# Optimization experiments

Hardware: AMD Instinct MI355X
Metric: run time of the kernel (lower is better)

The kernel has to match this reference:

```python
import jax, jax.numpy as jnp
import numpy as np

B, T, C = 1, 4096, 2048
NH, HS, NQG = 16, 128, 4          # n_head, head_size, n_query_groups (GQA)
Q_PER_KV = NH // NQG              # 4
QKV_DIM = (NH + 2 * NQG) * HS     # 3072
ROT = HS // 2                     # rotary half-dim = 64


def setup_inputs() -> dict:
    key = jax.random.key(0)
    k0, k1, k2 = jax.random.split(key, 3)
    x = jax.random.normal(k0, (B, T, C), dtype=jnp.float32)
    W_attn = jax.random.normal(k1, (QKV_DIM, C), dtype=jnp.float32) * 0.02
    W_proj = jax.random.normal(k2, (C, C), dtype=jnp.float32) * 0.02
    # RoPE cache: cos/sin of shape (T, head_size/2), flash-attn convention
    inv_freq = 1.0 / (10000.0 ** (jnp.arange(0, HS, 2, dtype=jnp.float32) / HS))
    freqs = jnp.arange(T, dtype=jnp.float32)[:, None] * inv_freq[None, :]
    return {"x": x, "cos": jnp.cos(freqs), "sin": jnp.sin(freqs),
            "W_attn": W_attn, "W_proj": W_proj}


def _apply_rope(t, cos, sin):
    # t: (B, T, H, HS); cos/sin: (T, ROT). Non-interleaved (rotate-half) form.
    x1, x2 = t[..., :ROT], t[..., ROT:]
    c = cos[None, :, None, :]
    s = sin[None, :, None, :]
    return jnp.concatenate([x1 * c - x2 * s, x2 * c + x1 * s], axis=-1)


def reference(x, cos, sin, W_attn, W_proj):
    Bx, Tx, Cx = x.shape
    qkv = jnp.einsum('btc,fc->btf', x, W_attn)                 # (B,T,3072)
    qkv = qkv.reshape(Bx, Tx, NQG, Q_PER_KV + 2, HS)
    q = qkv[:, :, :, :Q_PER_KV, :].reshape(Bx, Tx, NH, HS)     # (B,T,16,128)
    k = qkv[:, :, :, Q_PER_KV, :]                              # (B,T,4,128)
    v = qkv[:, :, :, Q_PER_KV + 1, :]                          # (B,T,4,128)
    q = _apply_rope(q, cos, sin)
    k = _apply_rope(k, cos, sin)
    # GQA: expand kv groups to match query heads (repeat_interleave on head dim)
    k = jnp.repeat(k, Q_PER_KV, axis=2)                        # (B,T,16,128)
    v = jnp.repeat(v, Q_PER_KV, axis=2)
    scale = 1.0 / np.sqrt(HS).astype(np.float32)
    scores = jnp.einsum('bthd,bshd->bhts', q, k) * scale       # (B,H,T,T)
    causal = jnp.tril(jnp.ones((Tx, Tx), dtype=bool))
    scores = jnp.where(causal[None, None], scores, jnp.finfo(scores.dtype).min)
    attn = jax.nn.softmax(scores, axis=-1)
    y = jnp.einsum('bhts,bshd->bthd', attn, v).reshape(Bx, Tx, Cx)
    return jnp.einsum('btc,oc->bto', y, W_proj)
```

## Files before the change

### kernel.cpp

```cpp
#include <hip/hip_runtime.h>
#include <hip/hip_bf16.h>

typedef __hip_bfloat16 bf16;
typedef __attribute__((ext_vector_type(8))) short short8;
typedef __attribute__((ext_vector_type(4))) short short4v;
typedef __attribute__((ext_vector_type(4))) float floatx4;

#define T_SEQ 4096
#define C_DIM 2048
#define NHEAD 16
#define HSZ   128
#define NGRP  4

#define MFMA_BF16(A,B,C) __builtin_amdgcn_mfma_f32_16x16x32_bf16((A),(B),(C),0,0,0)

__device__ __forceinline__ void gld_lds16(const bf16* g, bf16* l) {
  __builtin_amdgcn_global_load_lds(
      (__attribute__((address_space(1))) void*)(g),
      (__attribute__((address_space(3))) void*)(l), 16, 0, 0);
}

__global__ void cvt_kernel(const float* __restrict__ src, bf16* __restrict__ dst, long n)
{
  const long i = ((long)blockIdx.x * blockDim.x + threadIdx.x) * 8;
  if (i >= n) return;
  const float4 a = *(const float4*)(src + i);
  const float4 b = *(const float4*)(src + i + 4);
  bf16 tmp[8];
  tmp[0] = __float2bfloat16(a.x); tmp[1] = __float2bfloat16(a.y);
  tmp[2] = __float2bfloat16(a.z); tmp[3] = __float2bfloat16(a.w);
  tmp[4] = __float2bfloat16(b.x); tmp[5] = __float2bfloat16(b.y);
  tmp[6] = __float2bfloat16(b.z); tmp[7] = __float2bfloat16(b.w);
  *(short8*)(dst + i) = *(const short8*)tmp;
}

__global__ __launch_bounds__(256, 3)
void gemm_bt_kernel(const bf16* __restrict__ A, const bf16* __restrict__ B,
                    float* __restrict__ Cf, bf16* __restrict__ Cq,
                    bf16* __restrict__ Ck, bf16* __restrict__ Cvt,
                    const float* __restrict__ cs, const float* __restrict__ sn,
                    int K, int qkv_mode)
{
  __shared__ alignas(16) bf16 smem[128 * 132];
  bf16* As = smem;
  bf16* Bs = smem + 128 * 64;

  const int t  = threadIdx.x;
  const int w  = t >> 6, l = t & 63;
  const int wr = w >> 1, wc = w & 1;
  const int q4 = l >> 4, ln = l & 15;
  const long bm = (long)blockIdx.y * 128;
  const long bn = (long)blockIdx.x * 128;

  floatx4 acc[4][4] = {};

  const bf16* Ab = A + (bm + t / 8) * (long)K + (t % 8) * 8;
  const bf16* Bb = B + (bn + t / 8) * (long)K + (t % 8) * 8;

  for (int k0 = 0; k0 < K; k0 += 64) {
    __syncthreads();
#pragma unroll
    for (int i = 0; i < 4; ++i) {
      gld_lds16(Ab + (long)i * 32 * K + k0, As + (i * 256 + w * 64) * 8);
      gld_lds16(Bb + (long)i * 32 * K + k0, Bs + (i * 256 + w * 64) * 8);
    }
    __syncthreads();
#pragma unroll
    for (int kk = 0; kk < 64; kk += 32) {
      short8 af[4], bfr[4];
      const int co = kk + q4 * 8;
#pragma unroll
      for (int mi = 0; mi < 4; ++mi)
        af[mi] = *(const short8*)(As + (wr * 64 + mi * 16 + ln) * 64 + co);
#pragma unroll
      for (int ni = 0; ni < 4; ++ni)
        bfr[ni] = *(const short8*)(Bs + (wc * 64 + ni * 16 + ln) * 64 + co);
#pragma unroll
      for (int mi = 0; mi < 4; ++mi)
#pragma unroll
        for (int ni = 0; ni < 4; ++ni)
          acc[mi][ni] = MFMA_BF16(af[mi], bfr[ni], acc[mi][ni]);
    }
  }

  if (!qkv_mode) {
#pragma unroll
    for (int mi = 0; mi < 4; ++mi) {
      const long r0 = bm + wr * 64 + mi * 16 + q4 * 4;
#pragma unroll
      for (int ni = 0; ni < 4; ++ni) {
        const long c = bn + wc * 64 + ni * 16 + ln;
#pragma unroll
        for (int r = 0; r < 4; ++r)
          Cf[(r0 + r) * C_DIM + c] = acc[mi][ni][r];
      }
    }
  } else {
    const int cb = blockIdx.x;
    const int g = cb / 6, slot = cb - g * 6;
    if (slot == 5) {
      bf16* dstv = Cvt + (long)g * HSZ * T_SEQ;
#pragma unroll
      for (int pass = 0; pass < 2; ++pass) {
        __syncthreads();
        if (wc == pass) {
#pragma unroll
          for (int mi = 0; mi < 4; ++mi) {
            const int tc = wr * 64 + mi * 16 + q4 * 4;
#pragma unroll
            for (int ni = 0; ni < 4; ++ni) {
              const int dr = ni * 16 + ln;
              short4v pk;
#pragma unroll
              for (int r = 0; r < 4; ++r) {
                bf16 v = __float2bfloat16(acc[mi][ni][r]);
                pk[r] = *(short*)&v;
              }
              *(short4v*)(As + dr * 128 + tc) = pk;
            }
          }
        }
        __syncthreads();
        const int row = t >> 2, ch = (t & 3) * 32;
        bf16* gp = dstv + (long)(pass * 64 + row) * T_SEQ + bm + ch;
#pragma unroll
        for (int jj = 0; jj < 4; ++jj)
          *(short8*)(gp + jj * 8) = *(const short8*)(As + row * 128 + ch + jj * 8);
      }
    } else {
      bf16* dst = (slot < 4) ? (Cq + (long)(g * 4 + slot) * T_SEQ * HSZ)
                             : (Ck + (long)g * T_SEQ * HSZ);
      const float qs = (slot < 4) ? (0.08838834764831845f * 1.4426950408889634f) : 1.0f;
      __syncthreads();
      bf16* Ts = smem;
#pragma unroll
      for (int mi = 0; mi < 4; ++mi) {
        const int tl0 = wr * 64 + mi * 16 + q4 * 4;
#pragma unroll
        for (int ni = 0; ni < 4; ++ni) {
          const int cc = wc * 64 + ni * 16 + ln;
#pragma unroll
          for (int r = 0; r < 4; ++r)
            Ts[(tl0 + r) * 132 + cc] = __float2bfloat16(acc[mi][ni][r]);
        }
      }
      __syncthreads();
      const int tl = t >> 1, d0 = (t & 1) * 32;
      const long trow = bm + tl;
      bf16* gp = dst + trow * HSZ;
#pragma unroll
      for (int dj = 0; dj < 4; ++dj) {
        const int d = d0 + dj * 8;
        const short8 v1 = *(const short8*)(Ts + tl * 132 + d);
        const short8 v2 = *(const short8*)(Ts + tl * 132 + d + 64);
        const float4 c0 = *(const float4*)(cs + trow * 64 + d);
        const float4 c1 = *(const float4*)(cs + trow * 64 + d + 4);
        const float4 s0 = *(const float4*)(sn + trow * 64 + d);
        const float4 s1 = *(const float4*)(sn + trow * 64 + d + 4);
        const float ccv[8] = {c0.x,c0.y,c0.z,c0.w,c1.x,c1.y,c1.z,c1.w};
        const float ssv[8] = {s0.x,s0.y,s0.z,s0.w,s1.x,s1.y,s1.z,s1.w};
        short8 o1, o2;
#pragma unroll
        for (int jj = 0; jj < 8; ++jj) {
          short u1 = v1[jj], u2 = v2[jj];
          const float x1 = __bfloat162float(*(bf16*)&u1);
          const float x2 = __bfloat162float(*(bf16*)&u2);
          bf16 y1 = __float2bfloat16((x1 * ccv[jj] - x2 * ssv[jj]) * qs);
          bf16 y2 = __float2bfloat16((x2 * ccv[jj] + x1 * ssv[jj]) * qs);
          o1[jj] = *(short*)&y1; o2[jj] = *(short*)&y2;
        }
        *(short8*)(gp + d) = o1;
        *(short8*)(gp + d + 64) = o2;
      }
    }
  }
}

__global__ __launch_bounds__(256, 2)
void attn_kernel(const bf16* __restrict__ Qg, const bf16* __restrict__ Kg,
                 const bf16* __restrict__ Vtg, bf16* __restrict__ Y,
                 bf16* __restrict__ Opart, float* __restrict__ Lpart)
{
  __shared__ alignas(16) bf16 Ks[64][132];
  __shared__ alignas(16) bf16 Vt[128][68];
  __shared__ alignas(16) bf16 Ps[128][68];

  const int id  = blockIdx.x;
  const int h   = id >> 5;
  const int r   = id & 31;
  const int c   = r >> 1;
  const int isA = r & 1;
  const int g   = h >> 2;

  const int t = threadIdx.x;
  const int w = t >> 6, l = t & 63;
  const int q4 = l >> 4, ln = l & 15;

  const bf16* Qh = Qg + (long)h * T_SEQ * HSZ;
  const bf16* Kh = Kg + (long)g * T_SEQ * HSZ;
  const bf16* Vh = Vtg + (long)g * HSZ * T_SEQ;

  short8 ones_f;
#pragma unroll
  for (int i = 0; i < 8; ++i) ones_f[i] = (ln == 0) ? (short)0x3F80 : (short)0;

  const int krow = t >> 4, kc = (t & 15) * 8;
  const int vrow = t >> 3, vc = (t & 7) * 8;

  const int nph = isA ? 2 : 1;
  for (int ph = 0; ph < nph; ++ph) {
    const int P      = (isA && ph == 0) ? c : (31 - c);
    const int jlo    = (isA && ph == 1) ? 33 : 0;
    const int jhi    = isA ? (ph == 0 ? (2 * c + 2) : (64 - 2 * c)) : 33;
    const bool direct = (isA && ph == 0);
    const int qbase  = P * 128 + w * 32;

    short8 qf[2][4];
#pragma unroll
    for (int mi = 0; mi < 2; ++mi) {
      const long row = qbase + mi * 16 + ln;
#pragma unroll
      for (int ks = 0; ks < 4; ++ks)
        qf[mi][ks] = *(const short8*)(Qh + row * HSZ + ks * 32 + q4 * 8);
    }

    floatx4 acc[2][8] = {};
    floatx4 acc_l[2] = {};

    short8 kpre[4], vpre[4];
    {
      const int sb = jlo * 64;
#pragma unroll
      for (int i = 0; i < 4; ++i) {
        kpre[i] = *(const short8*)(Kh + (long)(sb + krow + 16 * i) * HSZ + kc);
        vpre[i] = *(const short8*)(Vh + (long)(vrow + 32 * i) * T_SEQ + sb + vc);
      }
    }

    for (int j = jlo; j < jhi; ++j) {
      const int s0 = j * 64;
#pragma unroll
      for (int i = 0; i < 4; ++i) {
        *(short8*)(&Ks[krow + 16 * i][kc]) = kpre[i];
        *(short8*)(&Vt[vrow + 32 * i][vc]) = vpre[i];
      }
      __syncthreads();
      if (j + 1 < jhi) {
        const int s1 = s0 + 64;
#pragma unroll
        for (int i = 0; i < 4; ++i) {
          kpre[i] = *(const short8*)(Kh + (long)(s1 + krow + 16 * i) * HSZ + kc);
          vpre[i] = *(const short8*)(Vh + (long)(vrow + 32 * i) * T_SEQ + s1 + vc);
        }
      }

      floatx4 sacc[2][4] = {};
#pragma unroll
      for (int ks = 0; ks < 4; ++ks) {
        short8 kf[4];
#pragma unroll
        for (int ni = 0; ni < 4; ++ni)
          kf[ni] = *(const short8*)(&Ks[ni * 16 + ln][ks * 32 + q4 * 8]);
#pragma unroll
        for (int mi = 0; mi < 2; ++mi)
#pragma unroll
          for (int ni = 0; ni < 4; ++ni)
            sacc[mi][ni] = MFMA_BF16(qf[mi][ks], kf[ni], sacc[mi][ni]);
      }

#pragma unroll
      for (int mi = 0; mi < 2; ++mi) {
        const int base_m = qbase + mi * 16 + q4 * 4 - s0 - ln;
#pragma unroll
        for (int ni = 0; ni < 4; ++ni)
#pragma unroll
          for (int r2 = 0; r2 < 4; ++r2) {
            float pv = __builtin_amdgcn_exp2f(sacc[mi][ni][r2]);
            if (base_m + r2 - ni * 16 < 0) pv = 0.f;
            Ps[w * 32 + mi * 16 + q4 * 4 + r2][ni * 16 + ln] = __float2bfloat16(pv);
          }
      }

#pragma unroll
      for (int ks = 0; ks < 2; ++ks) {
        short8 pf[2], vf[8];
#pragma unroll
        for (int mi = 0; mi < 2; ++mi)
          pf[mi] = *(const short8*)(&Ps[w * 32 + mi * 16 + ln][ks * 32 + q4 * 8]);
#pragma unroll
        for (int nd = 0; nd < 8; ++nd)
          vf[nd] = *(const short8*)(&Vt[nd * 16 + ln][ks * 32 + q4 * 8]);
#pragma unroll
        for (int mi = 0; mi < 2; ++mi) {
          acc_l[mi] = MFMA_BF16(pf[mi], ones_f, acc_l[mi]);
#pragma unroll
          for (int nd = 0; nd < 8; ++nd)
            acc[mi][nd] = MFMA_BF16(pf[mi], vf[nd], acc[mi][nd]);
        }
      }
      __syncthreads();
    }

    if (direct) {
#pragma unroll
      for (int mi = 0; mi < 2; ++mi) {
#pragma unroll
        for (int r2 = 0; r2 < 4; ++r2) {
          const float lv = __shfl(acc_l[mi][r2], l & 48, 64);
          const float inv = (lv > 0.f) ? 1.f / lv : 0.f;
          const long tq = qbase + mi * 16 + q4 * 4 + r2;
#pragma unroll
          for (int nd = 0; nd < 8; ++nd)
            Y[tq * C_DIM + h * HSZ + nd * 16 + ln] = __float2bfloat16(acc[mi][nd][r2] * inv);
        }
      }
    } else {
      const int sidx = (h * 16 + (15 - c)) * 2 + isA;
      bf16* Op = Opart + (long)sidx * (128 * 128);
      float* Lp = Lpart + sidx * 128;
#pragma unroll
      for (int mi = 0; mi < 2; ++mi) {
#pragma unroll
        for (int r2 = 0; r2 < 4; ++r2) {
          const int row = w * 32 + mi * 16 + q4 * 4 + r2;
          if (ln == 0) Lp[row] = acc_l[mi][r2];
#pragma unroll
          for (int nd = 0; nd < 8; ++nd)
            Op[row * 128 + nd * 16 + ln] = __float2bfloat16(acc[mi][nd][r2]);
        }
      }
    }
  }
}

__global__ void combine_kernel(const bf16* __restrict__ Opart,
                               const float* __restrict__ Lpart,
                               bf16* __restrict__ Y)
{
  const int b = blockIdx.x;
  const int h = b >> 4, pp = b & 15;
  const bf16* O0 = Opart + (long)b * 2 * 16384;
  const bf16* O1 = O0 + 16384;
  const float* L0 = Lpart + b * 256;
  const float* L1 = L0 + 128;
  const long qb = (long)(pp + 16) * 128;
  const int t = threadIdx.x;
#pragma unroll
  for (int it = 0; it < 8; ++it) {
    const int idx = it * 2048 + t * 8;
    const int row = idx >> 7, d = idx & 127;
    const float lsum = L0[row] + L1[row];
    const float inv = (lsum > 0.f) ? 1.f / lsum : 0.f;
    const short8 a = *(const short8*)(O0 + idx);
    const short8 bb = *(const short8*)(O1 + idx);
    short8 o;
#pragma unroll
    for (int jj = 0; jj < 8; ++jj) {
      short ua = a[jj], ub = bb[jj];
      const float fa = __bfloat162float(*(bf16*)&ua);
      const float fb = __bfloat162float(*(bf16*)&ub);
      bf16 y = __float2bfloat16((fa + fb) * inv);
      o[jj] = *(short*)&y;
    }
    *(short8*)(Y + (qb + row) * C_DIM + h * HSZ + d) = o;
  }
}

extern "C" void kernel_launch(void* const* d_in, const int* in_sizes, int n_in,
                              void* d_out, int out_size, void* d_ws, size_t ws_size,
                              hipStream_t stream)
{
  const float* x  = (const float*)d_in[0];
  const float* cs = (const float*)d_in[1];
  const float* sn = (const float*)d_in[2];
  const float* Wa = (const float*)d_in[3];
  const float* Wp = (const float*)d_in[4];
  float* out = (float*)d_out;

  const long nx  = (long)T_SEQ * C_DIM;
  const long nwa = (long)(NHEAD + 2 * NGRP) * HSZ * C_DIM;
  const long nwp = (long)C_DIM * C_DIM;
  const long nqh = (long)NHEAD * T_SEQ * HSZ;
  const long nkg = (long)NGRP * T_SEQ * HSZ;

  const size_t need = (size_t)(nx + nwa + nqh + 2 * nkg + nqh) * sizeof(bf16);
  if (ws_size < need) return;

  bf16* xb  = (bf16*)d_ws;
  bf16* Wab = xb + nx;
  bf16* Q   = Wab + nwa;
  bf16* K   = Q + nqh;
  bf16* Vt  = K + nkg;
  bf16* Y   = Vt + nkg;
  bf16* Wpb = Q;
  bf16* Opart = xb;
  float* Lpart = (float*)Wab;

  cvt_kernel<<<(int)(nx  / 8 / 256), 256, 0, stream>>>(x,  xb,  nx);
  cvt_kernel<<<(int)(nwa / 8 / 256), 256, 0, stream>>>(Wa, Wab, nwa);
  gemm_bt_kernel<<<dim3(24, 32), 256, 0, stream>>>(xb, Wab, nullptr, Q, K, Vt, cs, sn, C_DIM, 1);
  attn_kernel<<<512, 256, 0, stream>>>(Q, K, Vt, Y, Opart, Lpart);
  combine_kernel<<<256, 256, 0, stream>>>(Opart, Lpart, Y);
  cvt_kernel<<<(int)(nwp / 8 / 256), 256, 0, stream>>>(Wp, Wpb, nwp);
  gemm_bt_kernel<<<dim3(16, 32), 256, 0, stream>>>(Y, Wpb, out, nullptr, nullptr, nullptr, nullptr, nullptr, C_DIM, 0);
}
```

Measured before the change: 335.2 us.

## Use 32x32 MFMA with transposed S so P stays in registers

```diff
diff --git a/kernel.cpp b/kernel.cpp
--- a/kernel.cpp
+++ b/kernel.cpp
@@ -5,6 +5,7 @@
 typedef __attribute__((ext_vector_type(8))) short short8;
 typedef __attribute__((ext_vector_type(4))) short short4v;
 typedef __attribute__((ext_vector_type(4))) float floatx4;
+typedef __attribute__((ext_vector_type(16))) float floatx16;
 
 #define T_SEQ 4096
 #define C_DIM 2048
@@ -13,11 +14,18 @@
 #define NGRP  4
 
 #define MFMA_BF16(A,B,C) __builtin_amdgcn_mfma_f32_16x16x32_bf16((A),(B),(C),0,0,0)
+#define MFMA32(A,B,C)    __builtin_amdgcn_mfma_f32_32x32x16_bf16((A),(B),(C),0,0,0)
 
 __device__ __forceinline__ void gld_lds16(const bf16* g, bf16* l) {
   __builtin_amdgcn_global_load_lds(
       (__attribute__((address_space(1))) void*)(g),
       (__attribute__((address_space(3))) void*)(l), 16, 0, 0);
+}
+
+__device__ __forceinline__ unsigned pkbf(float a, float b) {
+  bf16 x = __float2bfloat16(a), y = __float2bfloat16(b);
+  unsigned short ux = *(unsigned short*)&x, uy = *(unsigned short*)&y;
+  return ((unsigned)uy << 16) | ux;
 }
 
 __global__ void cvt_kernel(const float* __restrict__ src, bf16* __restrict__ dst, long n)
@@ -183,7 +191,6 @@
 {
   __shared__ alignas(16) bf16 Ks[64][132];
   __shared__ alignas(16) bf16 Vt[128][68];
-  __shared__ alignas(16) bf16 Ps[128][68];
 
   const int id  = blockIdx.x;
   const int h   = id >> 5;
@@ -194,15 +201,11 @@
 
   const int t = threadIdx.x;
   const int w = t >> 6, l = t & 63;
-  const int q4 = l >> 4, ln = l & 15;
+  const int q32 = l & 31, hi = l >> 5;
 
   const bf16* Qh = Qg + (long)h * T_SEQ * HSZ;
   const bf16* Kh = Kg + (long)g * T_SEQ * HSZ;
   const bf16* Vh = Vtg + (long)g * HSZ * T_SEQ;
-
-  short8 ones_f;
-#pragma unroll
-  for (int i = 0; i < 8; ++i) ones_f[i] = (ln == 0) ? (short)0x3F80 : (short)0;
 
   const int krow = t >> 4, kc = (t & 15) * 8;
   const int vrow = t >> 3, vc = (t & 7) * 8;
@@ -214,18 +217,15 @@
     const int jhi    = isA ? (ph == 0 ? (2 * c + 2) : (64 - 2 * c)) : 33;
     const bool direct = (isA && ph == 0);
     const int qbase  = P * 128 + w * 32;
-
-    short8 qf[2][4];
-#pragma unroll
-    for (int mi = 0; mi < 2; ++mi) {
-      const long row = qbase + mi * 16 + ln;
-#pragma unroll
-      for (int ks = 0; ks < 4; ++ks)
-        qf[mi][ks] = *(const short8*)(Qh + row * HSZ + ks * 32 + q4 * 8);
-    }
-
-    floatx4 acc[2][8] = {};
-    floatx4 acc_l[2] = {};
+    const int qrow   = qbase + q32;
+
+    short8 qf[8];
+#pragma unroll
+    for (int kd = 0; kd < 8; ++kd)
+      qf[kd] = *(const short8*)(Qh + (long)qrow * HSZ + kd * 16 + hi * 8);
+
+    floatx16 oacc[4] = {};
+    float lacc = 0.f;
 
     short8 kpre[4], vpre[4];
     {
@@ -254,80 +254,78 @@
         }
       }
 
-      floatx4 sacc[2][4] = {};
-#pragma unroll
-      for (int ks = 0; ks < 4; ++ks) {
-        short8 kf[4];
+      floatx16 st[2] = {};
+#pragma unroll
+      for (int kd = 0; kd < 8; ++kd) {
+        const short8 ka0 = *(const short8*)(&Ks[q32][kd * 16 + hi * 8]);
+        const short8 ka1 = *(const short8*)(&Ks[32 + q32][kd * 16 + hi * 8]);
+        st[0] = MFMA32(ka0, qf[kd], st[0]);
+        st[1] = MFMA32(ka1, qf[kd], st[1]);
+      }
+
+      const bool domask = (s0 + 63 > qbase);
+#pragma unroll
+      for (int si = 0; si < 2; ++si) {
+        float pe[16];
+#pragma unroll
+        for (int rr = 0; rr < 16; ++rr) {
+          float v = __builtin_amdgcn_exp2f(st[si][rr]);
+          if (domask) {
+            const int sg = s0 + si * 32 + (rr & 3) + 8 * (rr >> 2) + 4 * hi;
+            if (sg > qrow) v = 0.f;
+          }
+          pe[rr] = v;
+          lacc += v;
+        }
+#pragma unroll
+        for (int k2 = 0; k2 < 2; ++k2) {
+          const int ks = si * 2 + k2;
+          const int ub = 8 * k2;
+          const unsigned pw0 = pkbf(pe[ub + 0], pe[ub + 1]);
+          const unsigned pw1 = pkbf(pe[ub + 2], pe[ub + 3]);
+          const unsigned pw2 = pkbf(pe[ub + 4], pe[ub + 5]);
+          const unsigned pw3 = pkbf(pe[ub + 6], pe[ub + 7]);
+          const unsigned sx0 = (unsigned)__shfl_xor((int)(hi ? pw0 : pw2), 32, 64);
+          const unsigned sx1 = (unsigned)__shfl_xor((int)(hi ? pw1 : pw3), 32, 64);
+          union { unsigned u4[4]; short8 s8; } pa;
+          pa.u4[0] = hi ? sx0 : pw0;
+          pa.u4[1] = hi ? sx1 : pw1;
+          pa.u4[2] = hi ? pw2 : sx0;
+          pa.u4[3] = hi ? pw3 : sx1;
+#pragma unroll
+          for (int ni = 0; ni < 4; ++ni) {
+            const short8 vb = *(const short8*)(&Vt[ni * 32 + q32][ks * 16 + hi * 8]);
+            oacc[ni] = MFMA32(pa.s8, vb, oacc[ni]);
+          }
+        }
+      }
+      __syncthreads();
+    }
+
+    const float lt = lacc + __shfl_xor(lacc, 32, 64);
+
+    if (direct) {
+#pragma unroll
+      for (int rr = 0; rr < 16; ++rr) {
+        const int qloc = (rr & 3) + 8 * (rr >> 2) + 4 * hi;
+        const float dv = __shfl(lt, qloc, 64);
+        const float inv = (dv > 0.f) ? 1.f / dv : 0.f;
+        bf16* yp = Y + (long)(qbase + qloc) * C_DIM + h * HSZ + q32;
 #pragma unroll
         for (int ni = 0; ni < 4; ++ni)
-          kf[ni] = *(const short8*)(&Ks[ni * 16 + ln][ks * 32 + q4 * 8]);
-#pragma unroll
-        for (int mi = 0; mi < 2; ++mi)
-#pragma unroll
-          for (int ni = 0; ni < 4; ++ni)
-            sacc[mi][ni] = MFMA_BF16(qf[mi][ks], kf[ni], sacc[mi][ni]);
-      }
-
-#pragma unroll
-      for (int mi = 0; mi < 2; ++mi) {
-        const int base_m = qbase + mi * 16 + q4 * 4 - s0 - ln;
-#pragma unroll
-        for (int ni = 0; ni < 4; ++ni)
-#pragma unroll
-          for (int r2 = 0; r2 < 4; ++r2) {
-            float pv = __builtin_amdgcn_exp2f(sacc[mi][ni][r2]);
-            if (base_m + r2 - ni * 16 < 0) pv = 0.f;
-            Ps[w * 32 + mi * 16 + q4 * 4 + r2][ni * 16 + ln] = __float2bfloat16(pv);
-          }
-      }
-
-#pragma unroll
-      for (int ks = 0; ks < 2; ++ks) {
-        short8 pf[2], vf[8];
-#pragma unroll
-        for (int mi = 0; mi < 2; ++mi)
-          pf[mi] = *(const short8*)(&Ps[w * 32 + mi * 16 + ln][ks * 32 + q4 * 8]);
-#pragma unroll
-        for (int nd = 0; nd < 8; ++nd)
-          vf[nd] = *(const short8*)(&Vt[nd * 16 + ln][ks * 32 + q4 * 8]);
-#pragma unroll
-        for (int mi = 0; mi < 2; ++mi) {
-          acc_l[mi] = MFMA_BF16(pf[mi], ones_f, acc_l[mi]);
-#pragma unroll
-          for (int nd = 0; nd < 8; ++nd)
-            acc[mi][nd] = MFMA_BF16(pf[mi], vf[nd], acc[mi][nd]);
-        }
-      }
-      __syncthreads();
-    }
-
-    if (direct) {
-#pragma unroll
-      for (int mi = 0; mi < 2; ++mi) {
-#pragma unroll
-        for (int r2 = 0; r2 < 4; ++r2) {
-          const float lv = __shfl(acc_l[mi][r2], l & 48, 64);
-          const float inv = (lv > 0.f) ? 1.f / lv : 0.f;
-          const long tq = qbase + mi * 16 + q4 * 4 + r2;
-#pragma unroll
-          for (int nd = 0; nd < 8; ++nd)
-            Y[tq * C_DIM + h * HSZ + nd * 16 + ln] = __float2bfloat16(acc[mi][nd][r2] * inv);
-        }
+          yp[ni * 32] = __float2bfloat16(oacc[ni][rr] * inv);
       }
     } else {
       const int sidx = (h * 16 + (15 - c)) * 2 + isA;
       bf16* Op = Opart + (long)sidx * (128 * 128);
       float* Lp = Lpart + sidx * 128;
-#pragma unroll
-      for (int mi = 0; mi < 2; ++mi) {
-#pragma unroll
-        for (int r2 = 0; r2 < 4; ++r2) {
-          const int row = w * 32 + mi * 16 + q4 * 4 + r2;
-          if (ln == 0) Lp[row] = acc_l[mi][r2];
-#pragma unroll
-          for (int nd = 0; nd < 8; ++nd)
-            Op[row * 128 + nd * 16 + ln] = __float2bfloat16(acc[mi][nd][r2]);
-        }
+      if (hi == 0) Lp[w * 32 + q32] = lt;
+#pragma unroll
+      for (int rr = 0; rr < 16; ++rr) {
+        const int qloc = (rr & 3) + 8 * (rr >> 2) + 4 * hi;
+#pragma unroll
+        for (int ni = 0; ni < 4; ++ni)
+          Op[(w * 32 + qloc) * 128 + ni * 32 + q32] = __float2bfloat16(oacc[ni][rr]);
       }
     }
   }
```

Result: slower. 349.3 us (+4.2%).
